# Optimization experiments

Measured on AMD Instinct MI355X. Metric: run time of the kernel, lower is better.

The kernel has to match this reference:

```python
import math
import jax, jax.numpy as jnp
import numpy as np

H = 12  # n_heads
NEG = -1e9

def setup_inputs() -> dict:
    key = jax.random.key(0)
    ks = jax.random.split(key, 5)
    B, S, D = 1, 4096, 768
    x = jax.random.normal(ks[0], (B, S, D), dtype=jnp.float32)
    Wqkv = jax.random.normal(ks[1], (D, 3 * D), dtype=jnp.float32) * (1.0 / math.sqrt(D))
    bqkv = jnp.zeros((3 * D,), dtype=jnp.float32)
    Wout = jax.random.normal(ks[2], (D, D), dtype=jnp.float32) * (1.0 / math.sqrt(D))
    bout = jnp.zeros((D,), dtype=jnp.float32)
    rel_bias = jax.random.normal(ks[3], (H, S, S), dtype=jnp.float32) * 0.02
    # additive causal mask: 0 on/below diagonal, large negative above
    causal_mask = jnp.where(jnp.tril(jnp.ones((S, S), dtype=bool)), 0.0, NEG).astype(jnp.float32)
    return {"x": x, "Wqkv": Wqkv, "bqkv": bqkv, "Wout": Wout, "bout": bout,
            "rel_bias": rel_bias, "causal_mask": causal_mask}

def reference(x, Wqkv, bqkv, Wout, bout, rel_bias, causal_mask):
    B, S, D = x.shape
    hd = D // H
    qkv = x @ Wqkv + bqkv                      # [B,S,3D]
    q, k, v = jnp.split(qkv, 3, axis=-1)
    def heads(t):  # [B,S,D] -> [B,H,S,hd]
        return t.reshape(B, S, H, hd).transpose(0, 2, 1, 3)
    q, k, v = heads(q), heads(k), heads(v)
    scores = jnp.einsum('bhqd,bhkd->bhqk', q, k) / math.sqrt(hd)
    scores = scores + rel_bias[None] + causal_mask[None, None]
    attn = jax.nn.softmax(scores, axis=-1)     # dropout p=0.0 -> identity
    out = jnp.einsum('bhqk,bhkd->bhqd', attn, v)
    out = out.transpose(0, 2, 1, 3).reshape(B, S, D)
    return out @ Wout + bout
```

## Files before the change

kernel.cpp:

```cpp
#include <hip/hip_runtime.h>
#include <stdint.h>

typedef _Float16 f16;
typedef _Float16 f16x8 __attribute__((ext_vector_type(8)));
typedef _Float16 f16x4 __attribute__((ext_vector_type(4)));
typedef float f32x4 __attribute__((ext_vector_type(4)));

#define NEGF -1e30f

static __device__ __forceinline__ f32x4 mfma16(f16x8 a, f16x8 b, f32x4 c) {
    return __builtin_amdgcn_mfma_f32_16x16x32_f16(a, b, c, 0, 0, 0);
}

static __device__ __forceinline__ void gload_lds16(const void* g, void* l) {
    __builtin_amdgcn_global_load_lds(
        (const __attribute__((address_space(1))) unsigned int*)g,
        (__attribute__((address_space(3))) unsigned int*)l, 16, 0, 0);
}

__global__ void cast_f32_f16(const float* __restrict__ src, f16* __restrict__ dst, int n) {
    int idx = blockIdx.x * blockDim.x + threadIdx.x;
    int stride = gridDim.x * blockDim.x;
    for (int i = idx * 4; i < n; i += stride * 4) {
        float4 v = *(const float4*)(src + i);
        f16x4 h;
        h[0] = (f16)v.x; h[1] = (f16)v.y; h[2] = (f16)v.z; h[3] = (f16)v.w;
        *(f16x4*)(dst + i) = h;
    }
}

__global__ void transpose_cast(const float* __restrict__ src, f16* __restrict__ dst, int R, int C) {
    __shared__ float tile[32][33];
    const int c0 = blockIdx.x * 32, r0 = blockIdx.y * 32;
    const int tx = threadIdx.x & 31, ty = threadIdx.x >> 5;
#pragma unroll
    for (int i = 0; i < 32; i += 8)
        tile[ty + i][tx] = src[(size_t)(r0 + ty + i) * C + c0 + tx];
    __syncthreads();
#pragma unroll
    for (int i = 0; i < 32; i += 8)
        dst[(size_t)(c0 + ty + i) * R + r0 + tx] = (f16)tile[tx][ty + i];
}

template <int MODE>
__global__ void __launch_bounds__(256, 2)
gemm_f16(const f16* __restrict__ A, const f16* __restrict__ Bt,
         const float* __restrict__ bias,
         f16* __restrict__ Qb, f16* __restrict__ Kb, f16* __restrict__ Vtb,
         float* __restrict__ Cout, int K, int N) {
    __shared__ alignas(16) f16 As[128 * 32];
    __shared__ alignas(16) f16 Bs[128 * 32];
    const int t = threadIdx.x;
    const int lane = t & 63, wid = t >> 6;
    const int wm = wid >> 1, wn = wid & 1;
    const int lr = lane & 15, lg = lane >> 4;
    const int m0 = blockIdx.y * 128, n0 = blockIdx.x * 128;
    f32x4 acc[4][4] = {};
    for (int k0 = 0; k0 < K; k0 += 32) {
#pragma unroll
        for (int i = 0; i < 2; i++) {
            const int cc = t + i * 256;
            const int rr = cc >> 2, ch = cc & 3;
            gload_lds16(A + (size_t)(m0 + rr) * K + k0 + ch * 8, (f16*)As + cc * 8);
            gload_lds16(Bt + (size_t)(n0 + rr) * K + k0 + ch * 8, (f16*)Bs + cc * 8);
        }
        __syncthreads();
        f16x8 af[4], bf[4];
#pragma unroll
        for (int i = 0; i < 4; i++)
            af[i] = *(const f16x8*)(As + (wm * 64 + i * 16 + lr) * 32 + lg * 8);
#pragma unroll
        for (int j = 0; j < 4; j++)
            bf[j] = *(const f16x8*)(Bs + (wn * 64 + j * 16 + lr) * 32 + lg * 8);
#pragma unroll
        for (int i = 0; i < 4; i++)
#pragma unroll
            for (int j = 0; j < 4; j++)
                acc[i][j] = mfma16(af[i], bf[j], acc[i][j]);
        __syncthreads();
    }
#pragma unroll
    for (int i = 0; i < 4; i++) {
#pragma unroll
        for (int j = 0; j < 4; j++) {
            const int n_g = n0 + wn * 64 + j * 16 + lr;
            const float bv = bias[n_g];
#pragma unroll
            for (int jj = 0; jj < 4; jj++) {
                const int m_g = m0 + wm * 64 + i * 16 + lg * 4 + jj;
                const float val = acc[i][j][jj] + bv;
                if (MODE == 0) {
                    if (n_g < 768) {
                        Qb[(((n_g >> 6) * 4096) + m_g) * 64 + (n_g & 63)] = (f16)(val * 0.125f);
                    } else if (n_g < 1536) {
                        const int n2 = n_g - 768;
                        Kb[(((n2 >> 6) * 4096) + m_g) * 64 + (n2 & 63)] = (f16)val;
                    } else {
                        const int n2 = n_g - 1536;
                        Vtb[((n2 >> 6) * 64 + (n2 & 63)) * 4096 + m_g] = (f16)val;
                    }
                } else {
                    Cout[(size_t)m_g * N + n_g] = val;
                }
            }
        }
    }
}

__global__ void __launch_bounds__(256, 2)
attn_fwd(const f16* __restrict__ Qb, const f16* __restrict__ Kb,
         const f16* __restrict__ Vtb, const float* __restrict__ rel_bias,
         float* __restrict__ Opart, float* __restrict__ mpart, float* __restrict__ lpart) {
    __shared__ alignas(16) f16 Ks[64 * 64];
    __shared__ alignas(16) f16 Vs[64 * 64];
    __shared__ alignas(16) f16 Ps[4][64 * 72];
    __shared__ alignas(16) float fac[4][64];
    const int bid = blockIdx.x;
    const int h = bid / 72;
    int rr = bid % 72;
    int Q = 0;
    for (;;) { const int n = (Q + 2) >> 1; if (rr < n) break; rr -= n; ++Q; }
    const int c = rr;
    const int lo = c * 8;
    const int hi = min(lo + 8, 4 * Q + 4);

    const int t = threadIdx.x, lane = t & 63, wid = t >> 6;
    const int lr = lane & 15, lg = lane >> 4;
    const int g = 4 * Q + wid;
    const int q0w = g * 64;
    const f16* Qh = Qb + (size_t)h * 4096 * 64;
    const f16* Kh = Kb + (size_t)h * 4096 * 64;
    const f16* Vh = Vtb + (size_t)h * 64 * 4096;
    const float* rbh = rel_bias + (size_t)h * 4096 * 4096;

    f16x8 qf[4][2];
#pragma unroll
    for (int nf = 0; nf < 4; nf++)
#pragma unroll
        for (int kd = 0; kd < 2; kd++)
            qf[nf][kd] = *(const f16x8*)(Qh + (size_t)(q0w + nf * 16 + lr) * 64 + kd * 32 + lg * 8);

    f32x4 o[4][4] = {};
    float mrow[4] = {NEGF, NEGF, NEGF, NEGF};
    float lrow[4] = {0.f, 0.f, 0.f, 0.f};
    const int qmaxw = q0w + 63;

    for (int kt = lo; kt < hi; kt++) {
        const int kbase = kt * 64;
#pragma unroll
        for (int i = 0; i < 2; i++) {
            const int cc = t + i * 256;
            const int row = cc >> 3, off = (cc & 7) * 8;
            gload_lds16(Kh + (size_t)(kbase + row) * 64 + off, (f16*)Ks + cc * 8);
            gload_lds16(Vh + (size_t)row * 4096 + kbase + off, (f16*)Vs + cc * 8);
        }
        __syncthreads();
        if (kbase <= qmaxw) {
            f32x4 st[4][4] = {};
#pragma unroll
            for (int kd = 0; kd < 2; kd++) {
#pragma unroll
                for (int mf = 0; mf < 4; mf++) {
                    const f16x8 kf = *(const f16x8*)(Ks + (mf * 16 + lr) * 64 + kd * 32 + lg * 8);
#pragma unroll
                    for (int nf = 0; nf < 4; nf++)
                        st[mf][nf] = mfma16(kf, qf[nf][kd], st[mf][nf]);
                }
            }
#pragma unroll
            for (int nf = 0; nf < 4; nf++) {
                const int q_g = q0w + nf * 16 + lr;
                const float* rbrow = rbh + (size_t)q_g * 4096 + kbase;
                float mx = NEGF;
#pragma unroll
                for (int mf = 0; mf < 4; mf++) {
                    const float4 rb = *(const float4*)(rbrow + mf * 16 + lg * 4);
                    const float rbv[4] = {rb.x, rb.y, rb.z, rb.w};
#pragma unroll
                    for (int jj = 0; jj < 4; jj++) {
                        const int k_g = kbase + mf * 16 + lg * 4 + jj;
                        float v = st[mf][nf][jj] + rbv[jj];
                        v = (k_g > q_g) ? NEGF : v;
                        st[mf][nf][jj] = v;
                        mx = fmaxf(mx, v);
                    }
                }
                mx = fmaxf(mx, __shfl_xor(mx, 16));
                mx = fmaxf(mx, __shfl_xor(mx, 32));
                const float mnew = fmaxf(mrow[nf], mx);
                const float fscale = __expf(mrow[nf] - mnew);
                mrow[nf] = mnew;
                float rsum = 0.f;
#pragma unroll
                for (int mf = 0; mf < 4; mf++) {
                    f16x4 pv;
#pragma unroll
                    for (int jj = 0; jj < 4; jj++) {
                        const float p = __expf(st[mf][nf][jj] - mnew);
                        rsum += p;
                        pv[jj] = (f16)p;
                    }
                    *(f16x4*)(&Ps[wid][(nf * 16 + lr) * 72 + mf * 16 + lg * 4]) = pv;
                }
                rsum += __shfl_xor(rsum, 16);
                rsum += __shfl_xor(rsum, 32);
                lrow[nf] = lrow[nf] * fscale + rsum;
                if (lane < 16) fac[wid][nf * 16 + lr] = fscale;
            }
            asm volatile("s_waitcnt lgkmcnt(0)" ::: "memory");
#pragma unroll
            for (int mf2 = 0; mf2 < 4; mf2++) {
                const float4 fv = *(const float4*)&fac[wid][mf2 * 16 + lg * 4];
                const float fvv[4] = {fv.x, fv.y, fv.z, fv.w};
#pragma unroll
                for (int nf2 = 0; nf2 < 4; nf2++)
#pragma unroll
                    for (int jj = 0; jj < 4; jj++)
                        o[mf2][nf2][jj] *= fvv[jj];
            }
#pragma unroll
            for (int kk = 0; kk < 2; kk++) {
                f16x8 pa[4], vb[4];
#pragma unroll
                for (int mf2 = 0; mf2 < 4; mf2++)
                    pa[mf2] = *(const f16x8*)(&Ps[wid][(mf2 * 16 + lr) * 72 + kk * 32 + lg * 8]);
#pragma unroll
                for (int nf2 = 0; nf2 < 4; nf2++)
                    vb[nf2] = *(const f16x8*)(Vs + (nf2 * 16 + lr) * 64 + kk * 32 + lg * 8);
#pragma unroll
                for (int mf2 = 0; mf2 < 4; mf2++)
#pragma unroll
                    for (int nf2 = 0; nf2 < 4; nf2++)
                        o[mf2][nf2] = mfma16(pa[mf2], vb[nf2], o[mf2][nf2]);
            }
        }
        __syncthreads();
    }

    const int s = (h * 64 + g) * 8 + c;
    float* Op = Opart + (size_t)s * 4096;
#pragma unroll
    for (int mf2 = 0; mf2 < 4; mf2++)
#pragma unroll
        for (int nf2 = 0; nf2 < 4; nf2++)
#pragma unroll
            for (int jj = 0; jj < 4; jj++)
                Op[(mf2 * 16 + lg * 4 + jj) * 64 + nf2 * 16 + lr] = o[mf2][nf2][jj];
    if (lg == 0) {
#pragma unroll
        for (int nf = 0; nf < 4; nf++) {
            mpart[(size_t)s * 64 + nf * 16 + lr] = mrow[nf];
            lpart[(size_t)s * 64 + nf * 16 + lr] = lrow[nf];
        }
    }
}

__global__ void __launch_bounds__(256)
merge_norm(const float* __restrict__ Opart, const float* __restrict__ mpart,
           const float* __restrict__ lpart, f16* __restrict__ Ob) {
    const int g = blockIdx.x, h = blockIdx.y;
    const int nc = ((g >> 2) + 2) >> 1;
    const int t = threadIdx.x;
    const int row = t >> 2, cq = t & 3;
    const size_t base = (size_t)((h * 64 + g) * 8);
    float M = NEGF;
#pragma unroll
    for (int i = 0; i < 8; i++)
        if (i < nc) M = fmaxf(M, mpart[(base + i) * 64 + row]);
    float L = 0.f;
    float acc0[8] = {}, acc1[8] = {};
#pragma unroll
    for (int i = 0; i < 8; i++) {
        if (i < nc) {
            const float w = __expf(mpart[(base + i) * 64 + row] - M);
            L += w * lpart[(base + i) * 64 + row];
            const float4* Or = (const float4*)(Opart + (base + i) * 4096 + row * 64 + cq * 16);
            const float4 v0 = Or[0], v1 = Or[1], v2 = Or[2], v3 = Or[3];
            acc0[0] += w * v0.x; acc0[1] += w * v0.y; acc0[2] += w * v0.z; acc0[3] += w * v0.w;
            acc0[4] += w * v1.x; acc0[5] += w * v1.y; acc0[6] += w * v1.z; acc0[7] += w * v1.w;
            acc1[0] += w * v2.x; acc1[1] += w * v2.y; acc1[2] += w * v2.z; acc1[3] += w * v2.w;
            acc1[4] += w * v3.x; acc1[5] += w * v3.y; acc1[6] += w * v3.z; acc1[7] += w * v3.w;
        }
    }
    const float inv = 1.f / L;
    const int q = g * 64 + row;
    f16x8 o0, o1;
#pragma unroll
    for (int j = 0; j < 8; j++) { o0[j] = (f16)(acc0[j] * inv); o1[j] = (f16)(acc1[j] * inv); }
    *(f16x8*)(Ob + (size_t)q * 768 + h * 64 + cq * 16) = o0;
    *(f16x8*)(Ob + (size_t)q * 768 + h * 64 + cq * 16 + 8) = o1;
}

extern "C" void kernel_launch(void* const* d_in, const int* in_sizes, int n_in,
                              void* d_out, int out_size, void* d_ws, size_t ws_size,
                              hipStream_t stream) {
    const float* x = (const float*)d_in[0];
    const float* Wqkv = (const float*)d_in[1];
    const float* bqkv = (const float*)d_in[2];
    const float* Wout = (const float*)d_in[3];
    const float* bout = (const float*)d_in[4];
    const float* rel_bias = (const float*)d_in[5];
    float* out = (float*)d_out;

    f16* p = (f16*)d_ws;
    f16* xb = p;     p += (size_t)4096 * 768;
    f16* WqkvT = p;  p += (size_t)2304 * 768;
    f16* WoutT = p;  p += (size_t)768 * 768;
    f16* Qb = p;     p += (size_t)12 * 4096 * 64;
    f16* Kb = p;     p += (size_t)12 * 4096 * 64;
    f16* Vtb = p;    p += (size_t)12 * 4096 * 64;
    f16* Ob = p;     p += (size_t)4096 * 768;
    float* fp = (float*)p;
    float* Opart = fp;  fp += (size_t)6144 * 4096;
    float* mpart = fp;  fp += (size_t)6144 * 64;
    float* lpart = fp;  fp += (size_t)6144 * 64;

    cast_f32_f16<<<3072, 256, 0, stream>>>(x, xb, 4096 * 768);
    transpose_cast<<<dim3(2304 / 32, 768 / 32), 256, 0, stream>>>(Wqkv, WqkvT, 768, 2304);
    transpose_cast<<<dim3(768 / 32, 768 / 32), 256, 0, stream>>>(Wout, WoutT, 768, 768);
    gemm_f16<0><<<dim3(18, 32), 256, 0, stream>>>(xb, WqkvT, bqkv, Qb, Kb, Vtb, nullptr, 768, 2304);
    attn_fwd<<<dim3(864), 256, 0, stream>>>(Qb, Kb, Vtb, rel_bias, Opart, mpart, lpart);
    merge_norm<<<dim3(64, 12), 256, 0, stream>>>(Opart, mpart, lpart, Ob);
    gemm_f16<1><<<dim3(6, 32), 256, 0, stream>>>(Ob, WoutT, bout, nullptr, nullptr, nullptr, out, 768, 768);
}
```

Before: 235.4 us.

## Double-buffer K/V tiles, prefetch rel_bias, swizzle LDS, and store partials as fp16

The attention kernel now double-buffers K/V tiles in shared memory, issuing the next tile's global-to-LDS load right after the barrier, and drops the trailing barrier. It prefetches the next tile's rel_bias into registers and seeds the QK^T accumulators with it. K/V shared-memory accesses use an XOR swizzle to reduce bank conflicts. Partial outputs are stored as fp16 in transposed layout, and merge_norm is rewritten to precompute weights in shared memory. This cuts memory traffic and exposed load latency, at the cost of more registers and LDS (which may hurt occupancy) and lower precision in the partials.

Result: slower. 321.9 us (+36.7%).

```diff
diff --git a/kernel.cpp b/kernel.cpp
--- a/kernel.cpp
+++ b/kernel.cpp
@@ -110,9 +110,9 @@
 __global__ void __launch_bounds__(256, 2)
 attn_fwd(const f16* __restrict__ Qb, const f16* __restrict__ Kb,
          const f16* __restrict__ Vtb, const float* __restrict__ rel_bias,
-         float* __restrict__ Opart, float* __restrict__ mpart, float* __restrict__ lpart) {
-    __shared__ alignas(16) f16 Ks[64 * 64];
-    __shared__ alignas(16) f16 Vs[64 * 64];
+         f16* __restrict__ Opart, float* __restrict__ mpart, float* __restrict__ lpart) {
+    __shared__ alignas(16) f16 Ks[2][64 * 64];
+    __shared__ alignas(16) f16 Vs[2][64 * 64];
     __shared__ alignas(16) f16 Ps[4][64 * 72];
     __shared__ alignas(16) float fac[4][64];
     const int bid = blockIdx.x;
@@ -133,6 +133,18 @@
     const f16* Vh = Vtb + (size_t)h * 64 * 4096;
     const float* rbh = rel_bias + (size_t)h * 4096 * 4096;
 
+    auto stage = [&](int buf, int kt) {
+        const int kbase = kt * 64;
+#pragma unroll
+        for (int i = 0; i < 2; i++) {
+            const int cc = t + i * 256;
+            const int row = cc >> 3;
+            const int cswz = (((cc & 7) * 16) ^ ((row & 7) << 4)) >> 1;
+            gload_lds16(Kh + (size_t)(kbase + row) * 64 + cswz, (f16*)Ks[buf] + cc * 8);
+            gload_lds16(Vh + (size_t)row * 4096 + kbase + cswz, (f16*)Vs[buf] + cc * 8);
+        }
+    };
+
     f16x8 qf[4][2];
 #pragma unroll
     for (int nf = 0; nf < 4; nf++)
@@ -145,23 +157,33 @@
     float lrow[4] = {0.f, 0.f, 0.f, 0.f};
     const int qmaxw = q0w + 63;
 
+    stage(0, lo);
+    f32x4 rbv[4][4];
+#pragma unroll
+    for (int nf = 0; nf < 4; nf++)
+#pragma unroll
+        for (int mf = 0; mf < 4; mf++)
+            rbv[nf][mf] = *(const f32x4*)(rbh + (size_t)(q0w + nf * 16 + lr) * 4096 + lo * 64 + mf * 16 + lg * 4);
+
     for (int kt = lo; kt < hi; kt++) {
         const int kbase = kt * 64;
-#pragma unroll
-        for (int i = 0; i < 2; i++) {
-            const int cc = t + i * 256;
-            const int row = cc >> 3, off = (cc & 7) * 8;
-            gload_lds16(Kh + (size_t)(kbase + row) * 64 + off, (f16*)Ks + cc * 8);
-            gload_lds16(Vh + (size_t)row * 4096 + kbase + off, (f16*)Vs + cc * 8);
-        }
+        const int cur = (kt - lo) & 1;
         __syncthreads();
+        if (kt + 1 < hi) stage(cur ^ 1, kt + 1);
         if (kbase <= qmaxw) {
-            f32x4 st[4][4] = {};
+            f32x4 st[4][4];
+#pragma unroll
+            for (int mf = 0; mf < 4; mf++)
+#pragma unroll
+                for (int nf = 0; nf < 4; nf++)
+                    st[mf][nf] = rbv[nf][mf];
 #pragma unroll
             for (int kd = 0; kd < 2; kd++) {
 #pragma unroll
                 for (int mf = 0; mf < 4; mf++) {
-                    const f16x8 kf = *(const f16x8*)(Ks + (mf * 16 + lr) * 64 + kd * 32 + lg * 8);
+                    const int r = mf * 16 + lr;
+                    const int cf = ((kd * 64 + lg * 16) ^ ((r & 7) << 4)) >> 1;
+                    const f16x8 kf = *(const f16x8*)(&Ks[cur][r * 64 + cf]);
 #pragma unroll
                     for (int nf = 0; nf < 4; nf++)
                         st[mf][nf] = mfma16(kf, qf[nf][kd], st[mf][nf]);
@@ -170,16 +192,13 @@
 #pragma unroll
             for (int nf = 0; nf < 4; nf++) {
                 const int q_g = q0w + nf * 16 + lr;
-                const float* rbrow = rbh + (size_t)q_g * 4096 + kbase;
                 float mx = NEGF;
 #pragma unroll
                 for (int mf = 0; mf < 4; mf++) {
-                    const float4 rb = *(const float4*)(rbrow + mf * 16 + lg * 4);
-                    const float rbv[4] = {rb.x, rb.y, rb.z, rb.w};
 #pragma unroll
                     for (int jj = 0; jj < 4; jj++) {
                         const int k_g = kbase + mf * 16 + lg * 4 + jj;
-                        float v = st[mf][nf][jj] + rbv[jj];
+                        float v = st[mf][nf][jj];
                         v = (k_g > q_g) ? NEGF : v;
                         st[mf][nf][jj] = v;
                         mx = fmaxf(mx, v);
@@ -207,6 +226,14 @@
                 lrow[nf] = lrow[nf] * fscale + rsum;
                 if (lane < 16) fac[wid][nf * 16 + lr] = fscale;
             }
+            if (kt + 1 < hi && (kt + 1) * 64 <= qmaxw) {
+                const int kb2 = (kt + 1) * 64;
+#pragma unroll
+                for (int nf = 0; nf < 4; nf++)
+#pragma unroll
+                    for (int mf = 0; mf < 4; mf++)
+                        rbv[nf][mf] = *(const f32x4*)(rbh + (size_t)(q0w + nf * 16 + lr) * 4096 + kb2 + mf * 16 + lg * 4);
+            }
             asm volatile("s_waitcnt lgkmcnt(0)" ::: "memory");
 #pragma unroll
             for (int mf2 = 0; mf2 < 4; mf2++) {
@@ -225,8 +252,11 @@
                 for (int mf2 = 0; mf2 < 4; mf2++)
                     pa[mf2] = *(const f16x8*)(&Ps[wid][(mf2 * 16 + lr) * 72 + kk * 32 + lg * 8]);
 #pragma unroll
-                for (int nf2 = 0; nf2 < 4; nf2++)
-                    vb[nf2] = *(const f16x8*)(Vs + (nf2 * 16 + lr) * 64 + kk * 32 + lg * 8);
+                for (int nf2 = 0; nf2 < 4; nf2++) {
+                    const int r = nf2 * 16 + lr;
+                    const int cf = ((kk * 64 + lg * 16) ^ ((r & 7) << 4)) >> 1;
+                    vb[nf2] = *(const f16x8*)(&Vs[cur][r * 64 + cf]);
+                }
 #pragma unroll
                 for (int mf2 = 0; mf2 < 4; mf2++)
 #pragma unroll
@@ -234,18 +264,20 @@
                         o[mf2][nf2] = mfma16(pa[mf2], vb[nf2], o[mf2][nf2]);
             }
         }
-        __syncthreads();
     }
 
     const int s = (h * 64 + g) * 8 + c;
-    float* Op = Opart + (size_t)s * 4096;
-#pragma unroll
-    for (int mf2 = 0; mf2 < 4; mf2++)
-#pragma unroll
-        for (int nf2 = 0; nf2 < 4; nf2++)
-#pragma unroll
-            for (int jj = 0; jj < 4; jj++)
-                Op[(mf2 * 16 + lg * 4 + jj) * 64 + nf2 * 16 + lr] = o[mf2][nf2][jj];
+    f16* Op = Opart + (size_t)s * 4096;
+#pragma unroll
+    for (int mf2 = 0; mf2 < 4; mf2++) {
+#pragma unroll
+        for (int nf2 = 0; nf2 < 4; nf2++) {
+            f16x4 pv;
+#pragma unroll
+            for (int jj = 0; jj < 4; jj++) pv[jj] = (f16)o[mf2][nf2][jj];
+            *(f16x4*)(Op + (nf2 * 16 + lr) * 64 + mf2 * 16 + lg * 4) = pv;
+        }
+    }
     if (lg == 0) {
 #pragma unroll
         for (int nf = 0; nf < 4; nf++) {
@@ -256,39 +288,49 @@
 }
 
 __global__ void __launch_bounds__(256)
-merge_norm(const float* __restrict__ Opart, const float* __restrict__ mpart,
+merge_norm(const f16* __restrict__ Opart, const float* __restrict__ mpart,
            const float* __restrict__ lpart, f16* __restrict__ Ob) {
+    __shared__ float wls[8][64];
+    __shared__ float Linv[64];
     const int g = blockIdx.x, h = blockIdx.y;
     const int nc = ((g >> 2) + 2) >> 1;
+    const size_t sb = (size_t)(h * 64 + g) * 8;
     const int t = threadIdx.x;
-    const int row = t >> 2, cq = t & 3;
-    const size_t base = (size_t)((h * 64 + g) * 8);
-    float M = NEGF;
-#pragma unroll
-    for (int i = 0; i < 8; i++)
-        if (i < nc) M = fmaxf(M, mpart[(base + i) * 64 + row]);
-    float L = 0.f;
-    float acc0[8] = {}, acc1[8] = {};
+    if (t < 64) {
+        float M = NEGF;
+#pragma unroll
+        for (int i = 0; i < 8; i++)
+            if (i < nc) M = fmaxf(M, mpart[(sb + i) * 64 + t]);
+        float L = 0.f;
+#pragma unroll
+        for (int i = 0; i < 8; i++)
+            if (i < nc) {
+                const float w = __expf(mpart[(sb + i) * 64 + t] - M);
+                wls[i][t] = w;
+                L += w * lpart[(sb + i) * 64 + t];
+            }
+        Linv[t] = 1.f / L;
+    }
+    __syncthreads();
+    const int d = t & 63, q0 = (t >> 6) * 16;
+    float acc[16] = {};
 #pragma unroll
     for (int i = 0; i < 8; i++) {
         if (i < nc) {
-            const float w = __expf(mpart[(base + i) * 64 + row] - M);
-            L += w * lpart[(base + i) * 64 + row];
-            const float4* Or = (const float4*)(Opart + (base + i) * 4096 + row * 64 + cq * 16);
-            const float4 v0 = Or[0], v1 = Or[1], v2 = Or[2], v3 = Or[3];
-            acc0[0] += w * v0.x; acc0[1] += w * v0.y; acc0[2] += w * v0.z; acc0[3] += w * v0.w;
-            acc0[4] += w * v1.x; acc0[5] += w * v1.y; acc0[6] += w * v1.z; acc0[7] += w * v1.w;
-            acc1[0] += w * v2.x; acc1[1] += w * v2.y; acc1[2] += w * v2.z; acc1[3] += w * v2.w;
-            acc1[4] += w * v3.x; acc1[5] += w * v3.y; acc1[6] += w * v3.z; acc1[7] += w * v3.w;
-        }
-    }
-    const float inv = 1.f / L;
-    const int q = g * 64 + row;
-    f16x8 o0, o1;
-#pragma unroll
-    for (int j = 0; j < 8; j++) { o0[j] = (f16)(acc0[j] * inv); o1[j] = (f16)(acc1[j] * inv); }
-    *(f16x8*)(Ob + (size_t)q * 768 + h * 64 + cq * 16) = o0;
-    *(f16x8*)(Ob + (size_t)q * 768 + h * 64 + cq * 16 + 8) = o1;
+            const f16x8 a = *(const f16x8*)(Opart + (sb + i) * 4096 + d * 64 + q0);
+            const f16x8 b = *(const f16x8*)(Opart + (sb + i) * 4096 + d * 64 + q0 + 8);
+#pragma unroll
+            for (int j = 0; j < 8; j++) {
+                acc[j] += wls[i][q0 + j] * (float)a[j];
+                acc[8 + j] += wls[i][q0 + 8 + j] * (float)b[j];
+            }
+        }
+    }
+#pragma unroll
+    for (int j = 0; j < 16; j++) {
+        const int q = g * 64 + q0 + j;
+        Ob[(size_t)q * 768 + h * 64 + d] = (f16)(acc[j] * Linv[q0 + j]);
+    }
 }
 
 extern "C" void kernel_launch(void* const* d_in, const int* in_sizes, int n_in,
@@ -310,8 +352,8 @@
     f16* Kb = p;     p += (size_t)12 * 4096 * 64;
     f16* Vtb = p;    p += (size_t)12 * 4096 * 64;
     f16* Ob = p;     p += (size_t)4096 * 768;
+    f16* Opart = p;  p += (size_t)6144 * 4096;
     float* fp = (float*)p;
-    float* Opart = fp;  fp += (size_t)6144 * 4096;
     float* mpart = fp;  fp += (size_t)6144 * 64;
     float* lpart = fp;  fp += (size_t)6144 * 64;
 
```

## Swizzle K/V shared-memory layout and store attention partials in fp16

Applied to the files above, without the earlier changes.

Applies an XOR swizzle to the K and V tiles in shared memory, on both the global-to-LDS load and the fragment reads, to reduce bank conflicts. It also stores the per-split unnormalized attention outputs as fp16 instead of fp32. That halves the write traffic from attn_fwd and the read traffic in merge_norm. Storing unnormalized partial sums in fp16 risks some precision loss or overflow.

New measurement: 227.1 us. 3.5% less time.

```diff
diff --git a/kernel.cpp b/kernel.cpp
--- a/kernel.cpp
+++ b/kernel.cpp
@@ -110,7 +110,7 @@
 __global__ void __launch_bounds__(256, 2)
 attn_fwd(const f16* __restrict__ Qb, const f16* __restrict__ Kb,
          const f16* __restrict__ Vtb, const float* __restrict__ rel_bias,
-         float* __restrict__ Opart, float* __restrict__ mpart, float* __restrict__ lpart) {
+         f16* __restrict__ Opart, float* __restrict__ mpart, float* __restrict__ lpart) {
     __shared__ alignas(16) f16 Ks[64 * 64];
     __shared__ alignas(16) f16 Vs[64 * 64];
     __shared__ alignas(16) f16 Ps[4][64 * 72];
@@ -150,9 +150,10 @@
 #pragma unroll
         for (int i = 0; i < 2; i++) {
             const int cc = t + i * 256;
-            const int row = cc >> 3, off = (cc & 7) * 8;
-            gload_lds16(Kh + (size_t)(kbase + row) * 64 + off, (f16*)Ks + cc * 8);
-            gload_lds16(Vh + (size_t)row * 4096 + kbase + off, (f16*)Vs + cc * 8);
+            const int row = cc >> 3;
+            const int cswz = (((cc & 7) * 16) ^ ((row & 7) << 4)) >> 1;
+            gload_lds16(Kh + (size_t)(kbase + row) * 64 + cswz, (f16*)Ks + cc * 8);
+            gload_lds16(Vh + (size_t)row * 4096 + kbase + cswz, (f16*)Vs + cc * 8);
         }
         __syncthreads();
         if (kbase <= qmaxw) {
@@ -161,7 +162,9 @@
             for (int kd = 0; kd < 2; kd++) {
 #pragma unroll
                 for (int mf = 0; mf < 4; mf++) {
-                    const f16x8 kf = *(const f16x8*)(Ks + (mf * 16 + lr) * 64 + kd * 32 + lg * 8);
+                    const int r = mf * 16 + lr;
+                    const int cf = ((kd * 64 + lg * 16) ^ ((r & 7) << 4)) >> 1;
+                    const f16x8 kf = *(const f16x8*)(Ks + r * 64 + cf);
 #pragma unroll
                     for (int nf = 0; nf < 4; nf++)
                         st[mf][nf] = mfma16(kf, qf[nf][kd], st[mf][nf]);
@@ -225,8 +228,11 @@
                 for (int mf2 = 0; mf2 < 4; mf2++)
                     pa[mf2] = *(const f16x8*)(&Ps[wid][(mf2 * 16 + lr) * 72 + kk * 32 + lg * 8]);
 #pragma unroll
-                for (int nf2 = 0; nf2 < 4; nf2++)
-                    vb[nf2] = *(const f16x8*)(Vs + (nf2 * 16 + lr) * 64 + kk * 32 + lg * 8);
+                for (int nf2 = 0; nf2 < 4; nf2++) {
+                    const int r = nf2 * 16 + lr;
+                    const int cf = ((kk * 64 + lg * 16) ^ ((r & 7) << 4)) >> 1;
+                    vb[nf2] = *(const f16x8*)(Vs + r * 64 + cf);
+                }
 #pragma unroll
                 for (int mf2 = 0; mf2 < 4; mf2++)
 #pragma unroll
@@ -238,14 +244,14 @@
     }
 
     const int s = (h * 64 + g) * 8 + c;
-    float* Op = Opart + (size_t)s * 4096;
+    f16* Op = Opart + (size_t)s * 4096;
 #pragma unroll
     for (int mf2 = 0; mf2 < 4; mf2++)
 #pragma unroll
         for (int nf2 = 0; nf2 < 4; nf2++)
 #pragma unroll
             for (int jj = 0; jj < 4; jj++)
-                Op[(mf2 * 16 + lg * 4 + jj) * 64 + nf2 * 16 + lr] = o[mf2][nf2][jj];
+                Op[(mf2 * 16 + lg * 4 + jj) * 64 + nf2 * 16 + lr] = (f16)o[mf2][nf2][jj];
     if (lg == 0) {
 #pragma unroll
         for (int nf = 0; nf < 4; nf++) {
@@ -256,7 +262,7 @@
 }
 
 __global__ void __launch_bounds__(256)
-merge_norm(const float* __restrict__ Opart, const float* __restrict__ mpart,
+merge_norm(const f16* __restrict__ Opart, const float* __restrict__ mpart,
            const float* __restrict__ lpart, f16* __restrict__ Ob) {
     const int g = blockIdx.x, h = blockIdx.y;
     const int nc = ((g >> 2) + 2) >> 1;
@@ -274,12 +280,13 @@
         if (i < nc) {
             const float w = __expf(mpart[(base + i) * 64 + row] - M);
             L += w * lpart[(base + i) * 64 + row];
-            const float4* Or = (const float4*)(Opart + (base + i) * 4096 + row * 64 + cq * 16);
-            const float4 v0 = Or[0], v1 = Or[1], v2 = Or[2], v3 = Or[3];
-            acc0[0] += w * v0.x; acc0[1] += w * v0.y; acc0[2] += w * v0.z; acc0[3] += w * v0.w;
-            acc0[4] += w * v1.x; acc0[5] += w * v1.y; acc0[6] += w * v1.z; acc0[7] += w * v1.w;
-            acc1[0] += w * v2.x; acc1[1] += w * v2.y; acc1[2] += w * v2.z; acc1[3] += w * v2.w;
-            acc1[4] += w * v3.x; acc1[5] += w * v3.y; acc1[6] += w * v3.z; acc1[7] += w * v3.w;
+            const f16x8 a = *(const f16x8*)(Opart + (base + i) * 4096 + row * 64 + cq * 16);
+            const f16x8 b = *(const f16x8*)(Opart + (base + i) * 4096 + row * 64 + cq * 16 + 8);
+#pragma unroll
+            for (int j = 0; j < 8; j++) {
+                acc0[j] += w * (float)a[j];
+                acc1[j] += w * (float)b[j];
+            }
         }
     }
     const float inv = 1.f / L;
@@ -310,8 +317,8 @@
     f16* Kb = p;     p += (size_t)12 * 4096 * 64;
     f16* Vtb = p;    p += (size_t)12 * 4096 * 64;
     f16* Ob = p;     p += (size_t)4096 * 768;
+    f16* Opart = p;  p += (size_t)6144 * 4096;
     float* fp = (float*)p;
-    float* Opart = fp;  fp += (size_t)6144 * 4096;
     float* mpart = fp;  fp += (size_t)6144 * 64;
     float* lpart = fp;  fp += (size_t)6144 * 64;
 
```
